# Optimization experiments

Measured on AMD Instinct MI355X. Metric: run time of the kernel, lower is better.

The kernel has to match this reference:

```python
import jax, jax.numpy as jnp
import numpy as np
from jax import lax

RWKV_K_CLAMP = 60.0
RWKV_K_EPS = 1e-8


def setup_inputs() -> dict:
    key = jax.random.key(0)
    ks = jax.random.split(key, 12)
    B, T, C = 4, 1024, 1024
    s = 1.0 / np.sqrt(C)  # scaled linear weights so exp(k) stays sane
    return {
        "xq": jax.random.normal(ks[0], (B, T, C), jnp.float32),
        "xk": jax.random.normal(ks[1], (B, T, C), jnp.float32),
        "xv": jax.random.normal(ks[2], (B, T, C), jnp.float32),
        "time_decay": jax.random.normal(ks[3], (C, 1), jnp.float32) * 0.1,
        "time_first": jnp.full((C, 1), np.log(0.3), jnp.float32),
        "time_mix_k": jax.random.uniform(ks[4], (1, 1, C), jnp.float32),
        "time_mix_v": jax.random.uniform(ks[5], (1, 1, C), jnp.float32),
        "time_mix_r": jax.random.uniform(ks[6], (1, 1, C), jnp.float32),
        "Wk": jax.random.normal(ks[7], (C, C), jnp.float32) * s,
        "Wv": jax.random.normal(ks[8], (C, C), jnp.float32) * s,
        "Wr": jax.random.normal(ks[9], (C, C), jnp.float32) * s,
        "Wo": jax.random.normal(ks[10], (C, C), jnp.float32) * s,
    }


def reference(xq, xk, xv, time_decay, time_first, time_mix_k, time_mix_v,
              time_mix_r, Wk, Wv, Wr, Wo):
    B, T, C = xq.shape
    x = xq  # module only uses xq
    # time_shift: ZeroPad2d((0,0,1,-1)) -> xx[t] = x[t-1], xx[0] = 0
    xx = jnp.pad(x, ((0, 0), (1, 0), (0, 0)))[:, :T]
    k = jnp.einsum('btc,dc->btd', x * time_mix_k + xx * (1 - time_mix_k), Wk)
    v = jnp.einsum('btc,dc->btd', x * time_mix_v + xx * (1 - time_mix_v), Wv)
    r = jnp.einsum('btc,dc->btd', x * time_mix_r + xx * (1 - time_mix_r), Wr)
    sr = jax.nn.sigmoid(r)

    kc = jnp.exp(jnp.minimum(k, RWKV_K_CLAMP)).transpose(0, 2, 1)  # [B,C,T]
    vc = v.transpose(0, 2, 1)                                       # [B,C,T]
    kv = kc * vc

    # time_curve (ctx_len == T): [-(T-2), ..., -1, 0], length T-1
    curve = jnp.arange(T - 1, dtype=jnp.float32) - (T - 2)
    time_w = jnp.concatenate(
        [jnp.exp(time_decay) * curve[None, :], time_first], axis=-1)  # [C,T]
    w = jnp.exp(time_w)[:, None, :]  # conv kernel [C,1,T]

    def dconv(a):  # causal grouped conv1d (torch conv1d == cross-correlation)
        ap = jnp.pad(a, ((0, 0), (0, 0), (T - 1, 0)))
        return lax.conv_general_dilated(
            ap, w, (1,), 'VALID', feature_group_count=C,
            dimension_numbers=('NCH', 'OIH', 'NCH'))

    wkv = dconv(kv)
    wk = dconv(kc) + RWKV_K_EPS
    out = sr * (wkv / wk).transpose(0, 2, 1)  # [B,T,C]
    return jnp.einsum('btc,dc->btd', out, Wo)
```

## Files before the change

### kernel.cpp

```cpp
#include <hip/hip_runtime.h>
#include <math.h>

constexpr int B = 4, T = 1024, C = 1024, D = 1024;
constexpr int M = B * T;
constexpr float K_CLAMP = 60.0f, K_EPS = 1e-8f;

typedef _Float16 half8 __attribute__((ext_vector_type(8)));
typedef _Float16 half4v __attribute__((ext_vector_type(4)));
typedef float float4v __attribute__((ext_vector_type(4)));

typedef __attribute__((address_space(3))) unsigned int lds_uint;
typedef const __attribute__((address_space(1))) unsigned int g_uint;
__device__ __forceinline__ void load_lds16(const void* g, void* l) {
    __builtin_amdgcn_global_load_lds((g_uint*)(size_t)g,
                                     (lds_uint*)(unsigned int)(size_t)l, 16, 0, 0);
}

__device__ __forceinline__ float fast_sigmoid(float v) {
    return __builtin_amdgcn_rcpf(1.0f + __expf(-v));
}

__global__ __launch_bounds__(256) void prep_kernel(
    const float* __restrict__ x, const float* __restrict__ tmk,
    const float* __restrict__ tmv, const float* __restrict__ tmr,
    _Float16* __restrict__ ak, _Float16* __restrict__ av, _Float16* __restrict__ ar)
{
    const int gid = blockIdx.x * 256 + threadIdx.x;
    const int m = gid >> 8;
    const int cg = (gid & 255) << 2;
    const int t = m & (T - 1);
    float4 xv = *(const float4*)(x + (size_t)m * C + cg);
    float4 xp = make_float4(0.f, 0.f, 0.f, 0.f);
    if (t != 0) xp = *(const float4*)(x + (size_t)(m - 1) * C + cg);
    float4 k4 = *(const float4*)(tmk + cg);
    float4 v4 = *(const float4*)(tmv + cg);
    float4 r4 = *(const float4*)(tmr + cg);
    half4v ok, ov, orr;
    ok[0] = (_Float16)(xv.x * k4.x + xp.x * (1.f - k4.x));
    ok[1] = (_Float16)(xv.y * k4.y + xp.y * (1.f - k4.y));
    ok[2] = (_Float16)(xv.z * k4.z + xp.z * (1.f - k4.z));
    ok[3] = (_Float16)(xv.w * k4.w + xp.w * (1.f - k4.w));
    ov[0] = (_Float16)(xv.x * v4.x + xp.x * (1.f - v4.x));
    ov[1] = (_Float16)(xv.y * v4.y + xp.y * (1.f - v4.y));
    ov[2] = (_Float16)(xv.z * v4.z + xp.z * (1.f - v4.z));
    ov[3] = (_Float16)(xv.w * v4.w + xp.w * (1.f - v4.w));
    orr[0] = (_Float16)(xv.x * r4.x + xp.x * (1.f - r4.x));
    orr[1] = (_Float16)(xv.y * r4.y + xp.y * (1.f - r4.y));
    orr[2] = (_Float16)(xv.z * r4.z + xp.z * (1.f - r4.z));
    orr[3] = (_Float16)(xv.w * r4.w + xp.w * (1.f - r4.w));
    *(half4v*)(ak + (size_t)m * C + cg) = ok;
    *(half4v*)(av + (size_t)m * C + cg) = ov;
    *(half4v*)(ar + (size_t)m * C + cg) = orr;
}

__global__ __launch_bounds__(256) void wcvt_kernel(
    const float* __restrict__ w0, const float* __restrict__ w1,
    const float* __restrict__ w2, const float* __restrict__ w3,
    _Float16* __restrict__ h0, _Float16* __restrict__ h1,
    _Float16* __restrict__ h2, _Float16* __restrict__ h3)
{
    const int mat = blockIdx.y;
    const float* s = mat == 0 ? w0 : mat == 1 ? w1 : mat == 2 ? w2 : w3;
    _Float16* d = mat == 0 ? h0 : mat == 1 ? h1 : mat == 2 ? h2 : h3;
    const int gid = blockIdx.x * 256 + threadIdx.x;
    float4 v = *(const float4*)(s + (size_t)gid * 4);
    half4v o;
    o[0] = (_Float16)v.x; o[1] = (_Float16)v.y;
    o[2] = (_Float16)v.z; o[3] = (_Float16)v.w;
    *(half4v*)(d + (size_t)gid * 4) = o;
}

__global__ __launch_bounds__(256) void gemm_in_kernel(
    const _Float16* __restrict__ ak, const _Float16* __restrict__ av, const _Float16* __restrict__ ar,
    const _Float16* __restrict__ wk, const _Float16* __restrict__ wv, const _Float16* __restrict__ wr,
    _Float16* __restrict__ kc, _Float16* __restrict__ vv, _Float16* __restrict__ sr)
{
    __shared__ _Float16 lA[128 * 64];
    __shared__ _Float16 lB[128 * 64];
    const int tid = threadIdx.x, wave = tid >> 6, lane = tid & 63;
    const int quad = lane >> 4, l15 = lane & 15;
    const int wm = wave & 1, wn = wave >> 1;
    const int mat = blockIdx.y >> 3;
    const int ntile = (blockIdx.y & 7) * 128;
    const int mtile = blockIdx.x * 128;
    const _Float16* A = (mat == 0 ? ak : mat == 1 ? av : ar) + (size_t)mtile * C;
    const _Float16* W = (mat == 0 ? wk : mat == 1 ? wv : wr) + (size_t)ntile * C;

    const int rS = tid >> 3, oS = tid & 7, cS = (oS - rS) & 7;
    const _Float16* pA = A + (size_t)rS * C + cS * 8;
    const _Float16* pB = W + (size_t)rS * C + cS * 8;

    int aOff[4], bOff[4];
#pragma unroll
    for (int i = 0; i < 4; i++) {
        int mm = wm * 64 + i * 16 + l15;
        aOff[i] = mm * 64 + (((quad + mm) & 7) << 3);
        int nn = wn * 64 + i * 16 + l15;
        bOff[i] = nn * 64 + (((quad + nn) & 7) << 3);
    }

    float4v acc[4][4] = {};
    for (int it = 0; it < 16; it++) {
#pragma unroll
        for (int n = 0; n < 4; n++) {
            load_lds16(pA + (size_t)n * 32 * C, lA + (n * 256 + wave * 64) * 8);
            load_lds16(pB + (size_t)n * 32 * C, lB + (n * 256 + wave * 64) * 8);
        }
        pA += 64; pB += 64;
        __syncthreads();
        half8 af[4], bf[4];
#pragma unroll
        for (int i = 0; i < 4; i++) af[i] = *(const half8*)(lA + aOff[i]);
#pragma unroll
        for (int j = 0; j < 4; j++) bf[j] = *(const half8*)(lB + bOff[j]);
#pragma unroll
        for (int i = 0; i < 4; i++)
#pragma unroll
            for (int j = 0; j < 4; j++)
                acc[i][j] = __builtin_amdgcn_mfma_f32_16x16x32_f16(af[i], bf[j], acc[i][j], 0, 0, 0);
#pragma unroll
        for (int i = 0; i < 4; i++) af[i] = *(const half8*)(lA + (aOff[i] ^ 32));
#pragma unroll
        for (int j = 0; j < 4; j++) bf[j] = *(const half8*)(lB + (bOff[j] ^ 32));
#pragma unroll
        for (int i = 0; i < 4; i++)
#pragma unroll
            for (int j = 0; j < 4; j++)
                acc[i][j] = __builtin_amdgcn_mfma_f32_16x16x32_f16(af[i], bf[j], acc[i][j], 0, 0, 0);
        __syncthreads();
    }

    const int bidx = mtile >> 10;
    const int tbase = (mtile & (T - 1)) + wm * 64;
    _Float16* Y = mat == 0 ? kc : mat == 1 ? vv : sr;
#pragma unroll
    for (int i = 0; i < 4; i++) {
#pragma unroll
        for (int j = 0; j < 4; j++) {
            const int d = ntile + wn * 64 + j * 16 + l15;
            const int t0 = tbase + i * 16 + quad * 4;
            half4v o;
#pragma unroll
            for (int r = 0; r < 4; r++) {
                float v = acc[i][j][r];
                if (mat == 0) v = __expf(fminf(v, K_CLAMP));
                else if (mat == 2) v = fast_sigmoid(v);
                o[r] = (_Float16)v;
            }
            *(half4v*)(Y + (((size_t)(bidx * D + d)) << 10) + t0) = o;
        }
    }
}

__global__ __launch_bounds__(256) void gemm_out_kernel(
    const _Float16* __restrict__ midT, const _Float16* __restrict__ wo,
    float* __restrict__ out)
{
    __shared__ _Float16 lA[64 * 64];
    __shared__ _Float16 lB[128 * 64];
    const int tid = threadIdx.x, wave = tid >> 6, lane = tid & 63;
    const int quad = lane >> 4, l15 = lane & 15;
    const int wm = wave & 1, wn = wave >> 1;
    const int mtile = blockIdx.x * 64;
    const int ntile = blockIdx.y * 128;
    const _Float16* A = midT + (size_t)mtile * C;
    const _Float16* W = wo + (size_t)ntile * C;

    const int rS = tid >> 3, oS = tid & 7, cS = (oS - rS) & 7;
    const _Float16* pA = A + (size_t)rS * C + cS * 8;
    const _Float16* pB = W + (size_t)rS * C + cS * 8;

    int aOff[2], bOff[4];
#pragma unroll
    for (int i = 0; i < 2; i++) {
        int mm = wm * 32 + i * 16 + l15;
        aOff[i] = mm * 64 + (((quad + mm) & 7) << 3);
    }
#pragma unroll
    for (int j = 0; j < 4; j++) {
        int nn = wn * 64 + j * 16 + l15;
        bOff[j] = nn * 64 + (((quad + nn) & 7) << 3);
    }

    float4v acc[2][4] = {};
    for (int it = 0; it < 16; it++) {
#pragma unroll
        for (int n = 0; n < 2; n++)
            load_lds16(pA + (size_t)n * 32 * C, lA + (n * 256 + wave * 64) * 8);
#pragma unroll
        for (int n = 0; n < 4; n++)
            load_lds16(pB + (size_t)n * 32 * C, lB + (n * 256 + wave * 64) * 8);
        pA += 64; pB += 64;
        __syncthreads();
        half8 af[2], bf[4];
#pragma unroll
        for (int i = 0; i < 2; i++) af[i] = *(const half8*)(lA + aOff[i]);
#pragma unroll
        for (int j = 0; j < 4; j++) bf[j] = *(const half8*)(lB + bOff[j]);
#pragma unroll
        for (int i = 0; i < 2; i++)
#pragma unroll
            for (int j = 0; j < 4; j++)
                acc[i][j] = __builtin_amdgcn_mfma_f32_16x16x32_f16(af[i], bf[j], acc[i][j], 0, 0, 0);
#pragma unroll
        for (int i = 0; i < 2; i++) af[i] = *(const half8*)(lA + (aOff[i] ^ 32));
#pragma unroll
        for (int j = 0; j < 4; j++) bf[j] = *(const half8*)(lB + (bOff[j] ^ 32));
#pragma unroll
        for (int i = 0; i < 2; i++)
#pragma unroll
            for (int j = 0; j < 4; j++)
                acc[i][j] = __builtin_amdgcn_mfma_f32_16x16x32_f16(af[i], bf[j], acc[i][j], 0, 0, 0);
        __syncthreads();
    }
#pragma unroll
    for (int i = 0; i < 2; i++) {
#pragma unroll
        for (int j = 0; j < 4; j++) {
            const int dcol = ntile + wn * 64 + j * 16 + l15;
#pragma unroll
            for (int r = 0; r < 4; r++) {
                const int m = mtile + wm * 32 + i * 16 + quad * 4 + r;
                out[(size_t)m * D + dcol] = acc[i][j][r];
            }
        }
    }
}

__global__ __launch_bounds__(256) void scan_kernel(
    const _Float16* __restrict__ kc, const _Float16* __restrict__ vv,
    const _Float16* __restrict__ sr, const float* __restrict__ td,
    const float* __restrict__ tf, _Float16* __restrict__ mid)
{
    const int gtid = blockIdx.x * 256 + threadIdx.x;
    const int wave = gtid >> 6;
    const int lane = threadIdx.x & 63;
    const int c = wave & (C - 1);
    const int bidx = wave >> 10;
    const float wfac = expf(-expf(td[c]));
    const float ef = expf(tf[c]);
    const size_t base = (((size_t)(bidx * C + c)) << 10) + lane * 16;

    half8 kA = *(const half8*)(kc + base), kB = *(const half8*)(kc + base + 8);
    half8 vA = *(const half8*)(vv + base), vB = *(const half8*)(vv + base + 8);
    half8 sA = *(const half8*)(sr + base), sB = *(const half8*)(sr + base + 8);
    float kcl[16], vl[16], srl[16];
#pragma unroll
    for (int i = 0; i < 8; i++) {
        kcl[i] = (float)kA[i]; kcl[8 + i] = (float)kB[i];
        vl[i]  = (float)vA[i]; vl[8 + i]  = (float)vB[i];
        srl[i] = (float)sA[i]; srl[8 + i] = (float)sB[i];
    }
    float ua = 0.f, ub = 0.f;
#pragma unroll
    for (int i = 0; i < 16; i++) {
        float kv = kcl[i] * vl[i];
        ua = fmaf(wfac, ua, kv);
        ub = fmaf(wfac, ub, kcl[i]);
    }
    float w2 = wfac * wfac, w4 = w2 * w2, w8 = w4 * w4, w16 = w8 * w8;
    float f = w16, sa = ua, sb = ub;
#pragma unroll
    for (int off = 1; off < 64; off <<= 1) {
        float pa = __shfl_up(sa, off);
        float pb = __shfl_up(sb, off);
        if (lane >= off) { sa = fmaf(f, pa, sa); sb = fmaf(f, pb, sb); }
        f = f * f;
    }
    float a0 = __shfl_up(sa, 1);
    float b0 = __shfl_up(sb, 1);
    if (lane == 0) { a0 = 0.f; b0 = 0.f; }
    half8 o0, o1;
#pragma unroll
    for (int i = 0; i < 16; i++) {
        float kv = kcl[i] * vl[i];
        float wkv = fmaf(ef, kv, a0);
        float wk = fmaf(ef, kcl[i], b0) + K_EPS;
        float o = srl[i] * (wkv / wk);
        if (i < 8) o0[i] = (_Float16)o; else o1[i - 8] = (_Float16)o;
        a0 = fmaf(wfac, a0, kv);
        b0 = fmaf(wfac, b0, kcl[i]);
    }
    *(half8*)(mid + base) = o0;
    *(half8*)(mid + base + 8) = o1;
}

__global__ __launch_bounds__(256) void transpose_kernel(
    const _Float16* __restrict__ mid, _Float16* __restrict__ midT)
{
    __shared__ _Float16 tile[64][72];
    const int b = blockIdx.z;
    const int ct = blockIdx.y * 64;
    const int tt = blockIdx.x * 64;
    const int tid = threadIdx.x;
#pragma unroll
    for (int it = 0; it < 2; it++) {
        const int cc = (tid >> 3) + it * 32;
        const int t8 = (tid & 7) * 8;
        half8 v = *(const half8*)(mid + (((size_t)(b * C + ct + cc)) << 10) + tt + t8);
#pragma unroll
        for (int j = 0; j < 8; j++) tile[t8 + j][cc] = v[j];
    }
    __syncthreads();
#pragma unroll
    for (int it = 0; it < 2; it++) {
        const int t = (tid >> 3) + it * 32;
        const int c8 = (tid & 7) * 8;
        half8 v;
#pragma unroll
        for (int j = 0; j < 8; j++) v[j] = tile[t][c8 + j];
        *(half8*)(midT + (((size_t)(b * T + tt + t)) << 10) + ct + c8) = v;
    }
}

extern "C" void kernel_launch(void* const* d_in, const int* in_sizes, int n_in,
                              void* d_out, int out_size, void* d_ws, size_t ws_size,
                              hipStream_t stream) {
    const float* xq  = (const float*)d_in[0];
    const float* td  = (const float*)d_in[3];
    const float* tf  = (const float*)d_in[4];
    const float* tmk = (const float*)d_in[5];
    const float* tmv = (const float*)d_in[6];
    const float* tmr = (const float*)d_in[7];
    const float* Wk  = (const float*)d_in[8];
    const float* Wv  = (const float*)d_in[9];
    const float* Wr  = (const float*)d_in[10];
    const float* Wo  = (const float*)d_in[11];
    float* out = (float*)d_out;

    const size_t MC = (size_t)M * C;
    char* ws = (char*)d_ws;
    _Float16* ak   = (_Float16*)(ws);
    _Float16* av   = (_Float16*)(ws + MC * 2);
    _Float16* ar   = (_Float16*)(ws + MC * 4);
    _Float16* wk16 = (_Float16*)(ws + MC * 6);
    _Float16* wv16 = wk16 + (size_t)D * C;
    _Float16* wr16 = wv16 + (size_t)D * C;
    _Float16* wo16 = wr16 + (size_t)D * C;
    _Float16* kc16 = (_Float16*)(ws + MC * 6 + (size_t)D * C * 8);
    _Float16* vv16 = kc16 + MC;
    _Float16* sr16 = vv16 + MC;
    _Float16* mid  = ak;
    _Float16* midT = av;

    prep_kernel<<<dim3(M * C / 4 / 256), dim3(256), 0, stream>>>(
        xq, tmk, tmv, tmr, ak, av, ar);
    wcvt_kernel<<<dim3(D * C / 4 / 256, 4), dim3(256), 0, stream>>>(
        Wk, Wv, Wr, Wo, wk16, wv16, wr16, wo16);
    gemm_in_kernel<<<dim3(M / 128, 24), dim3(256), 0, stream>>>(
        ak, av, ar, wk16, wv16, wr16, kc16, vv16, sr16);
    scan_kernel<<<dim3(B * C * 64 / 256), dim3(256), 0, stream>>>(
        kc16, vv16, sr16, td, tf, mid);
    transpose_kernel<<<dim3(T / 64, C / 64, B), dim3(256), 0, stream>>>(
        mid, midT);
    gemm_out_kernel<<<dim3(M / 64, D / 128), dim3(256), 0, stream>>>(
        midT, wo16, out);
}
```

Before: 188.1 us.

## Fuse conversion kernels, fold transpose into scan, stage GEMM epilogues via LDS

Merges the activation-prep and weight-conversion kernels into one launch and folds the transpose into the scan kernel, which now runs 16 channels per 1024-thread block and writes the time-major output through LDS. Both GEMM epilogues now stage their results in shared memory, so global stores become wide and coalesced instead of strided 4-element or scalar writes. This cuts two launches and one full round trip of the intermediate tensor through global memory. In exchange the GEMMs use more LDS and an extra barrier, and the scan blocks are large, which can reduce occupancy.

```diff
diff --git a/kernel.cpp b/kernel.cpp
--- a/kernel.cpp
+++ b/kernel.cpp
@@ -20,54 +20,55 @@
     return __builtin_amdgcn_rcpf(1.0f + __expf(-v));
 }
 
-__global__ __launch_bounds__(256) void prep_kernel(
+__global__ __launch_bounds__(256) void convert_kernel(
     const float* __restrict__ x, const float* __restrict__ tmk,
     const float* __restrict__ tmv, const float* __restrict__ tmr,
-    _Float16* __restrict__ ak, _Float16* __restrict__ av, _Float16* __restrict__ ar)
-{
-    const int gid = blockIdx.x * 256 + threadIdx.x;
-    const int m = gid >> 8;
-    const int cg = (gid & 255) << 2;
-    const int t = m & (T - 1);
-    float4 xv = *(const float4*)(x + (size_t)m * C + cg);
-    float4 xp = make_float4(0.f, 0.f, 0.f, 0.f);
-    if (t != 0) xp = *(const float4*)(x + (size_t)(m - 1) * C + cg);
-    float4 k4 = *(const float4*)(tmk + cg);
-    float4 v4 = *(const float4*)(tmv + cg);
-    float4 r4 = *(const float4*)(tmr + cg);
-    half4v ok, ov, orr;
-    ok[0] = (_Float16)(xv.x * k4.x + xp.x * (1.f - k4.x));
-    ok[1] = (_Float16)(xv.y * k4.y + xp.y * (1.f - k4.y));
-    ok[2] = (_Float16)(xv.z * k4.z + xp.z * (1.f - k4.z));
-    ok[3] = (_Float16)(xv.w * k4.w + xp.w * (1.f - k4.w));
-    ov[0] = (_Float16)(xv.x * v4.x + xp.x * (1.f - v4.x));
-    ov[1] = (_Float16)(xv.y * v4.y + xp.y * (1.f - v4.y));
-    ov[2] = (_Float16)(xv.z * v4.z + xp.z * (1.f - v4.z));
-    ov[3] = (_Float16)(xv.w * v4.w + xp.w * (1.f - v4.w));
-    orr[0] = (_Float16)(xv.x * r4.x + xp.x * (1.f - r4.x));
-    orr[1] = (_Float16)(xv.y * r4.y + xp.y * (1.f - r4.y));
-    orr[2] = (_Float16)(xv.z * r4.z + xp.z * (1.f - r4.z));
-    orr[3] = (_Float16)(xv.w * r4.w + xp.w * (1.f - r4.w));
-    *(half4v*)(ak + (size_t)m * C + cg) = ok;
-    *(half4v*)(av + (size_t)m * C + cg) = ov;
-    *(half4v*)(ar + (size_t)m * C + cg) = orr;
-}
-
-__global__ __launch_bounds__(256) void wcvt_kernel(
+    _Float16* __restrict__ ak, _Float16* __restrict__ av, _Float16* __restrict__ ar,
     const float* __restrict__ w0, const float* __restrict__ w1,
     const float* __restrict__ w2, const float* __restrict__ w3,
     _Float16* __restrict__ h0, _Float16* __restrict__ h1,
     _Float16* __restrict__ h2, _Float16* __restrict__ h3)
 {
-    const int mat = blockIdx.y;
-    const float* s = mat == 0 ? w0 : mat == 1 ? w1 : mat == 2 ? w2 : w3;
-    _Float16* d = mat == 0 ? h0 : mat == 1 ? h1 : mat == 2 ? h2 : h3;
-    const int gid = blockIdx.x * 256 + threadIdx.x;
-    float4 v = *(const float4*)(s + (size_t)gid * 4);
-    half4v o;
-    o[0] = (_Float16)v.x; o[1] = (_Float16)v.y;
-    o[2] = (_Float16)v.z; o[3] = (_Float16)v.w;
-    *(half4v*)(d + (size_t)gid * 4) = o;
+    const int bid = blockIdx.x;
+    if (bid < 4096) {
+        const int gid = bid * 256 + threadIdx.x;
+        const int m = gid >> 8;
+        const int cg = (gid & 255) << 2;
+        const int t = m & (T - 1);
+        float4 xv = *(const float4*)(x + (size_t)m * C + cg);
+        float4 xp = make_float4(0.f, 0.f, 0.f, 0.f);
+        if (t != 0) xp = *(const float4*)(x + (size_t)(m - 1) * C + cg);
+        float4 k4 = *(const float4*)(tmk + cg);
+        float4 v4 = *(const float4*)(tmv + cg);
+        float4 r4 = *(const float4*)(tmr + cg);
+        half4v ok, ov, orr;
+        ok[0] = (_Float16)(xv.x * k4.x + xp.x * (1.f - k4.x));
+        ok[1] = (_Float16)(xv.y * k4.y + xp.y * (1.f - k4.y));
+        ok[2] = (_Float16)(xv.z * k4.z + xp.z * (1.f - k4.z));
+        ok[3] = (_Float16)(xv.w * k4.w + xp.w * (1.f - k4.w));
+        ov[0] = (_Float16)(xv.x * v4.x + xp.x * (1.f - v4.x));
+        ov[1] = (_Float16)(xv.y * v4.y + xp.y * (1.f - v4.y));
+        ov[2] = (_Float16)(xv.z * v4.z + xp.z * (1.f - v4.z));
+        ov[3] = (_Float16)(xv.w * v4.w + xp.w * (1.f - v4.w));
+        orr[0] = (_Float16)(xv.x * r4.x + xp.x * (1.f - r4.x));
+        orr[1] = (_Float16)(xv.y * r4.y + xp.y * (1.f - r4.y));
+        orr[2] = (_Float16)(xv.z * r4.z + xp.z * (1.f - r4.z));
+        orr[3] = (_Float16)(xv.w * r4.w + xp.w * (1.f - r4.w));
+        *(half4v*)(ak + (size_t)m * C + cg) = ok;
+        *(half4v*)(av + (size_t)m * C + cg) = ov;
+        *(half4v*)(ar + (size_t)m * C + cg) = orr;
+    } else {
+        const int q = bid - 4096;
+        const int mat = q >> 10;
+        const float* s = mat == 0 ? w0 : mat == 1 ? w1 : mat == 2 ? w2 : w3;
+        _Float16* d = mat == 0 ? h0 : mat == 1 ? h1 : mat == 2 ? h2 : h3;
+        const int gid = (q & 1023) * 256 + threadIdx.x;
+        float4 v = *(const float4*)(s + (size_t)gid * 4);
+        half4v o;
+        o[0] = (_Float16)v.x; o[1] = (_Float16)v.y;
+        o[2] = (_Float16)v.z; o[3] = (_Float16)v.w;
+        *(half4v*)(d + (size_t)gid * 4) = o;
+    }
 }
 
 __global__ __launch_bounds__(256) void gemm_in_kernel(
@@ -75,8 +76,9 @@
     const _Float16* __restrict__ wk, const _Float16* __restrict__ wv, const _Float16* __restrict__ wr,
     _Float16* __restrict__ kc, _Float16* __restrict__ vv, _Float16* __restrict__ sr)
 {
-    __shared__ _Float16 lA[128 * 64];
-    __shared__ _Float16 lB[128 * 64];
+    __shared__ _Float16 lds[16896];
+    _Float16* lA = lds;
+    _Float16* lB = lds + 8192;
     const int tid = threadIdx.x, wave = tid >> 6, lane = tid & 63;
     const int quad = lane >> 4, l15 = lane & 15;
     const int wm = wave & 1, wn = wave >> 1;
@@ -130,15 +132,12 @@
         __syncthreads();
     }
 
-    const int bidx = mtile >> 10;
-    const int tbase = (mtile & (T - 1)) + wm * 64;
-    _Float16* Y = mat == 0 ? kc : mat == 1 ? vv : sr;
 #pragma unroll
     for (int i = 0; i < 4; i++) {
 #pragma unroll
         for (int j = 0; j < 4; j++) {
-            const int d = ntile + wn * 64 + j * 16 + l15;
-            const int t0 = tbase + i * 16 + quad * 4;
+            const int dl = wn * 64 + j * 16 + l15;
+            const int tl = wm * 64 + i * 16 + quad * 4;
             half4v o;
 #pragma unroll
             for (int r = 0; r < 4; r++) {
@@ -147,8 +146,19 @@
                 else if (mat == 2) v = fast_sigmoid(v);
                 o[r] = (_Float16)v;
             }
-            *(half4v*)(Y + (((size_t)(bidx * D + d)) << 10) + t0) = o;
+            *(half4v*)(lds + dl * 132 + tl) = o;
         }
+    }
+    __syncthreads();
+    const int bidx = mtile >> 10;
+    const int tglob0 = mtile & (T - 1);
+    _Float16* Y = mat == 0 ? kc : mat == 1 ? vv : sr;
+#pragma unroll
+    for (int s = 0; s < 8; s++) {
+        const int cid = s * 256 + tid;
+        const int dl = cid >> 4, tc = (cid & 15) << 3;
+        half8 v = *(const half8*)(lds + dl * 132 + tc);
+        *(half8*)(Y + (((size_t)(bidx * D + ntile + dl)) << 10) + tglob0 + tc) = v;
     }
 }
 
@@ -156,8 +166,10 @@
     const _Float16* __restrict__ midT, const _Float16* __restrict__ wo,
     float* __restrict__ out)
 {
-    __shared__ _Float16 lA[64 * 64];
-    __shared__ _Float16 lB[128 * 64];
+    __shared__ __align__(16) char smem[33792];
+    _Float16* lA = (_Float16*)smem;
+    _Float16* lB = (_Float16*)(smem + 8192);
+    float* tileo = (float*)smem;
     const int tid = threadIdx.x, wave = tid >> 6, lane = tid & 63;
     const int quad = lane >> 4, l15 = lane & 15;
     const int wm = wave & 1, wn = wave >> 1;
@@ -217,29 +229,38 @@
     for (int i = 0; i < 2; i++) {
 #pragma unroll
         for (int j = 0; j < 4; j++) {
-            const int dcol = ntile + wn * 64 + j * 16 + l15;
+            const int dl = wn * 64 + j * 16 + l15;
 #pragma unroll
             for (int r = 0; r < 4; r++) {
-                const int m = mtile + wm * 32 + i * 16 + quad * 4 + r;
-                out[(size_t)m * D + dcol] = acc[i][j][r];
+                const int ml = wm * 32 + i * 16 + quad * 4 + r;
+                tileo[ml * 132 + dl] = acc[i][j][r];
             }
         }
     }
-}
-
-__global__ __launch_bounds__(256) void scan_kernel(
+    __syncthreads();
+#pragma unroll
+    for (int s = 0; s < 8; s++) {
+        const int cid = s * 256 + tid;
+        const int ml = cid >> 5, dc = (cid & 31) << 2;
+        float4 v = *(const float4*)(tileo + ml * 132 + dc);
+        *(float4*)(out + (size_t)(mtile + ml) * D + ntile + dc) = v;
+    }
+}
+
+__global__ __launch_bounds__(1024) void scan_tr_kernel(
     const _Float16* __restrict__ kc, const _Float16* __restrict__ vv,
     const _Float16* __restrict__ sr, const float* __restrict__ td,
-    const float* __restrict__ tf, _Float16* __restrict__ mid)
+    const float* __restrict__ tf, _Float16* __restrict__ midT)
 {
-    const int gtid = blockIdx.x * 256 + threadIdx.x;
-    const int wave = gtid >> 6;
-    const int lane = threadIdx.x & 63;
-    const int c = wave & (C - 1);
-    const int bidx = wave >> 10;
+    __shared__ _Float16 L[16 * 1026];
+    const int tid = threadIdx.x;
+    const int w = tid >> 6, lane = tid & 63;
+    const int bq = blockIdx.x >> 6;
+    const int c0 = (blockIdx.x & 63) << 4;
+    const int c = c0 + w;
     const float wfac = expf(-expf(td[c]));
     const float ef = expf(tf[c]);
-    const size_t base = (((size_t)(bidx * C + c)) << 10) + lane * 16;
+    const size_t base = (((size_t)(bq * C + c)) << 10) + lane * 16;
 
     half8 kA = *(const half8*)(kc + base), kB = *(const half8*)(kc + base + 8);
     half8 vA = *(const half8*)(vv + base), vB = *(const half8*)(vv + base + 8);
@@ -281,36 +302,17 @@
         a0 = fmaf(wfac, a0, kv);
         b0 = fmaf(wfac, b0, kcl[i]);
     }
-    *(half8*)(mid + base) = o0;
-    *(half8*)(mid + base + 8) = o1;
-}
-
-__global__ __launch_bounds__(256) void transpose_kernel(
-    const _Float16* __restrict__ mid, _Float16* __restrict__ midT)
-{
-    __shared__ _Float16 tile[64][72];
-    const int b = blockIdx.z;
-    const int ct = blockIdx.y * 64;
-    const int tt = blockIdx.x * 64;
-    const int tid = threadIdx.x;
-#pragma unroll
-    for (int it = 0; it < 2; it++) {
-        const int cc = (tid >> 3) + it * 32;
-        const int t8 = (tid & 7) * 8;
-        half8 v = *(const half8*)(mid + (((size_t)(b * C + ct + cc)) << 10) + tt + t8);
-#pragma unroll
-        for (int j = 0; j < 8; j++) tile[t8 + j][cc] = v[j];
-    }
+    *(half8*)(L + w * 1026 + lane * 16) = o0;
+    *(half8*)(L + w * 1026 + lane * 16 + 8) = o1;
     __syncthreads();
-#pragma unroll
-    for (int it = 0; it < 2; it++) {
-        const int t = (tid >> 3) + it * 32;
-        const int c8 = (tid & 7) * 8;
-        half8 v;
-#pragma unroll
-        for (int j = 0; j < 8; j++) v[j] = tile[t][c8 + j];
-        *(half8*)(midT + (((size_t)(b * T + tt + t)) << 10) + ct + c8) = v;
-    }
+    half8 g0, g1;
+#pragma unroll
+    for (int cc = 0; cc < 8; cc++)  g0[cc] = L[cc * 1026 + tid];
+#pragma unroll
+    for (int cc = 0; cc < 8; cc++)  g1[cc] = L[(cc + 8) * 1026 + tid];
+    _Float16* dst = midT + (((size_t)(bq * T + tid)) << 10) + c0;
+    *(half8*)(dst) = g0;
+    *(half8*)(dst + 8) = g1;
 }
 
 extern "C" void kernel_launch(void* const* d_in, const int* in_sizes, int n_in,
@@ -340,19 +342,14 @@
     _Float16* kc16 = (_Float16*)(ws + MC * 6 + (size_t)D * C * 8);
     _Float16* vv16 = kc16 + MC;
     _Float16* sr16 = vv16 + MC;
-    _Float16* mid  = ak;
-    _Float16* midT = av;
-
-    prep_kernel<<<dim3(M * C / 4 / 256), dim3(256), 0, stream>>>(
-        xq, tmk, tmv, tmr, ak, av, ar);
-    wcvt_kernel<<<dim3(D * C / 4 / 256, 4), dim3(256), 0, stream>>>(
-        Wk, Wv, Wr, Wo, wk16, wv16, wr16, wo16);
+    _Float16* midT = ak;
+
+    convert_kernel<<<dim3(8192), dim3(256), 0, stream>>>(
+        xq, tmk, tmv, tmr, ak, av, ar, Wk, Wv, Wr, Wo, wk16, wv16, wr16, wo16);
     gemm_in_kernel<<<dim3(M / 128, 24), dim3(256), 0, stream>>>(
         ak, av, ar, wk16, wv16, wr16, kc16, vv16, sr16);
-    scan_kernel<<<dim3(B * C * 64 / 256), dim3(256), 0, stream>>>(
-        kc16, vv16, sr16, td, tf, mid);
-    transpose_kernel<<<dim3(T / 64, C / 64, B), dim3(256), 0, stream>>>(
-        mid, midT);
+    scan_tr_kernel<<<dim3(B * C / 16), dim3(1024), 0, stream>>>(
+        kc16, vv16, sr16, td, tf, midT);
     gemm_out_kernel<<<dim3(M / 64, D / 128), dim3(256), 0, stream>>>(
         midT, wo16, out);
 }
```

After: 185.1 us. Within noise of the previous version (-1.6%).
